# Optimization experiments

Measured on AMD Instinct MI355X. Metric: run time of the kernel, lower is better.

Reference implementation:

```python
import jax, jax.numpy as jnp
import numpy as np

B, T, D, E, K = 4, 2048, 1024, 8, 2


def setup_inputs() -> dict:
    key = jax.random.key(0)
    k1, k2, k3 = jax.random.split(key, 3)
    x = jax.random.normal(k1, (B, T, D), dtype=jnp.float32)
    Wg = jax.random.normal(k2, (D, E), dtype=jnp.float32) * (1.0 / np.sqrt(D))
    # xavier_uniform for We: limit = sqrt(6/(D+D))
    lim = float(np.sqrt(6.0 / (D + D)))
    We = jax.random.uniform(k3, (E, D, D), dtype=jnp.float32, minval=-lim, maxval=lim)
    return {"x": x, "Wg": Wg, "We": We}


def reference(x, Wg, We):
    # gate: (B,T,E) softmax over experts
    logits = jnp.einsum('btd,de->bte', x, Wg)
    gate = jax.nn.softmax(logits, axis=-1)
    top_val, top_idx = jax.lax.top_k(gate, K)          # (B,T,K)
    top_w = top_val / (jnp.sum(top_val, axis=-1, keepdims=True) + 1e-9)
    # dense all-expert projection, as in the original module
    x_experts = jnp.einsum('btd,edm->btem', x, We)      # (B,T,E,D)
    # gather selected experts: (B,T,K,D)
    x_sel = jnp.take_along_axis(x_experts, top_idx[..., None], axis=2)
    out = jnp.sum(x_sel * top_w[..., None], axis=2)     # (B,T,D)
    return out
```

## Files before the change

### kernel.cpp

```cpp
#include <hip/hip_runtime.h>
#include <hip/hip_bf16.h>
#include <stdint.h>

#define NTOK 8192
#define D_   1024
#define E_   8
#define MT   128
#define NT   128
#define KSTEPS 32
#define MAX_TILES 96

#define LIM_F  0.05412658773652741f
#define SB_F   (LIM_F / 127.0f)
#define INVSB_F (127.0f / LIM_F)

typedef __attribute__((ext_vector_type(4))) int i32x4;

__device__ inline unsigned short f2b(float f) {
    unsigned int u = __float_as_uint(f);
    unsigned int r = (u + 0x7fffu + ((u >> 16) & 1u)) >> 16;
    return (unsigned short)r;
}
__device__ inline float b2f(unsigned short b) {
    return __uint_as_float(((unsigned)b) << 16);
}
__device__ inline int q8(float v, float inv) {
    int q = __float2int_rn(v * inv);
    return max(-127, min(127, q));
}

__device__ inline void gload16(const void* g, void* l) {
    __builtin_amdgcn_global_load_lds(
        (const __attribute__((address_space(1))) unsigned int*)(uintptr_t)g,
        (__attribute__((address_space(3))) unsigned int*)(unsigned int)(uintptr_t)l,
        16, 0, 0);
}

__global__ __launch_bounds__(256) void prep_kernel(const float* __restrict__ We,
                                                   unsigned char* __restrict__ WeT8,
                                                   const float* __restrict__ x,
                                                   const float* __restrict__ Wg,
                                                   int* __restrict__ g_tok,
                                                   float* __restrict__ wA_tok,
                                                   float* __restrict__ wB_tok,
                                                   float* __restrict__ sA_tok,
                                                   unsigned char* __restrict__ Abf8) {
    __shared__ __align__(16) float smem[8192];
    int b = blockIdx.x;
    int t = threadIdx.x;
    if (b < 1024) {
        float* wgt = smem;
        for (int i = t; i < 8192; i += 256) wgt[(i & 7) * 1024 + (i >> 3)] = Wg[i];
        __syncthreads();
        int wave = t >> 6, lane = t & 63;
        int tok0 = b * 8 + wave * 2;

        for (int tki = 0; tki < 2; tki++) {
            int tok = tok0 + tki;
            const float* xr = x + (size_t)tok * D_;

            float4 xv[4];
            float acc[8] = {0.f, 0.f, 0.f, 0.f, 0.f, 0.f, 0.f, 0.f};
            float ax = 0.f;
            #pragma unroll
            for (int i = 0; i < 4; i++) {
                int d0 = i * 256 + lane * 4;
                xv[i] = *reinterpret_cast<const float4*>(xr + d0);
                ax = fmaxf(ax, fmaxf(fmaxf(fabsf(xv[i].x), fabsf(xv[i].y)),
                                     fmaxf(fabsf(xv[i].z), fabsf(xv[i].w))));
                #pragma unroll
                for (int e = 0; e < 8; e++) {
                    float4 w = *reinterpret_cast<const float4*>(&wgt[e * 1024 + d0]);
                    acc[e] += xv[i].x * w.x + xv[i].y * w.y + xv[i].z * w.z + xv[i].w * w.w;
                }
            }
            #pragma unroll
            for (int off = 32; off > 0; off >>= 1) ax = fmaxf(ax, __shfl_xor(ax, off, 64));
            #pragma unroll
            for (int e = 0; e < 8; e++)
                #pragma unroll
                for (int off = 32; off > 0; off >>= 1)
                    acc[e] += __shfl_xor(acc[e], off, 64);

            float best = acc[0]; int bi = 0;
            #pragma unroll
            for (int e = 1; e < 8; e++) { if (acc[e] > best) { best = acc[e]; bi = e; } }
            float second = -3.4e38f; int si = 0;
            #pragma unroll
            for (int e = 0; e < 8; e++) { if (e != bi && acc[e] > second) { second = acc[e]; si = e; } }
            float eb = __expf(second - best);
            eb = fmaxf(eb, 1e-20f);
            float w0 = 1.f / (1.f + eb);
            float w1 = eb / (1.f + eb);
            int ea, ebx; float wA, wB;
            if (bi < si) { ea = bi; ebx = si; wA = w0; wB = w1; }
            else         { ea = si; ebx = bi; wA = w1; wB = w0; }
            float inv = (ax > 0.f) ? 127.f / ax : 0.f;
            if (lane == 0) {
                g_tok[tok] = ea * 8 + ebx;
                wA_tok[tok] = wA;
                wB_tok[tok] = wB;
                sA_tok[tok] = ax / 127.f;
            }

            unsigned char* rowp = Abf8 + (size_t)tok * D_;
            #pragma unroll
            for (int i = 0; i < 4; i++) {
                int d0 = i * 256 + lane * 4;
                int q0 = q8(xv[i].x, inv), q1 = q8(xv[i].y, inv);
                int q2 = q8(xv[i].z, inv), q3 = q8(xv[i].w, inv);
                unsigned p = (q0 & 0xff) | ((q1 & 0xff) << 8) | ((q2 & 0xff) << 16) | ((q3 & 0xff) << 24);
                *reinterpret_cast<unsigned*>(rowp + d0) = p;
            }
        }
    } else {
        float (*tile)[65] = reinterpret_cast<float (*)[65]>(smem);
        int bb = b - 1024;
        int e = bb >> 8, rem = bb & 255;
        int m0 = (rem & 15) * 64, d0 = (rem >> 4) * 64;
        const float* src = We + ((size_t)e << 20);
        int r = t >> 4, c4 = (t & 15) * 4;
        #pragma unroll
        for (int i = 0; i < 4; i++) {
            int d = r + i * 16;
            float4 v = *reinterpret_cast<const float4*>(src + (size_t)(d0 + d) * D_ + m0 + c4);
            tile[d][c4 + 0] = v.x; tile[d][c4 + 1] = v.y;
            tile[d][c4 + 2] = v.z; tile[d][c4 + 3] = v.w;
        }
        __syncthreads();
        int m = t >> 2, dq = (t & 3) * 16;
        unsigned pk[4];
        #pragma unroll
        for (int jq = 0; jq < 4; jq++) {
            int q0 = q8(tile[dq + jq * 4 + 0][m], INVSB_F);
            int q1 = q8(tile[dq + jq * 4 + 1][m], INVSB_F);
            int q2 = q8(tile[dq + jq * 4 + 2][m], INVSB_F);
            int q3 = q8(tile[dq + jq * 4 + 3][m], INVSB_F);
            pk[jq] = (q0 & 0xff) | ((q1 & 0xff) << 8) | ((q2 & 0xff) << 16) | ((q3 & 0xff) << 24);
        }
        *reinterpret_cast<uint4*>(WeT8 + ((size_t)e << 20) + (size_t)(m0 + m) * D_ + d0 + dq) =
            make_uint4(pk[0], pk[1], pk[2], pk[3]);
    }
}

__global__ __launch_bounds__(256) void route_kernel(const int* __restrict__ g_tok,
                                                    const float* __restrict__ wA_tok,
                                                    const float* __restrict__ wB_tok,
                                                    const float* __restrict__ sA_tok,
                                                    int* __restrict__ token_list,
                                                    float* __restrict__ wA_s,
                                                    float* __restrict__ wB_s,
                                                    float* __restrict__ sA_s,
                                                    int4* __restrict__ tile_desc,
                                                    int* __restrict__ n_tiles_out) {
    int g = blockIdx.x;
    int t = threadIdx.x;
    __shared__ int cnt[64];
    __shared__ int pfx[256];
    __shared__ int startg, tbase, tottiles;
    if (t < 64) cnt[t] = 0;
    __syncthreads();

    int base = t * 32;
    int gl[32];
    int my = 0;
    #pragma unroll
    for (int k = 0; k < 32; k++) {
        gl[k] = g_tok[base + k];
        my += (gl[k] == g);
    }
    #pragma unroll
    for (int k = 0; k < 32; k++) atomicAdd(&cnt[gl[k]], 1);
    pfx[t] = my;
    __syncthreads();

    if (t == 0) {
        int run = 0, tb = 0, tt = 0;
        for (int gg = 0; gg < 64; gg++) {
            int c = cnt[gg];
            int n = 0, rem = c;
            while (rem > 64) { int take = (rem >= 128) ? 128 : rem; rem -= take; n++; }
            if (rem > 0) n++;
            if (gg < g) { run += c; tb += n; }
            tt += n;
        }
        startg = run; tbase = tb; tottiles = tt;
    }
    for (int off = 1; off < 256; off <<= 1) {
        int add = (t >= off) ? pfx[t - off] : 0;
        __syncthreads();
        pfx[t] += add;
        __syncthreads();
    }

    int pos = startg + pfx[t] - my;
    #pragma unroll
    for (int k = 0; k < 32; k++) {
        if (gl[k] == g) {
            int idx = base + k;
            token_list[pos] = idx;
            wA_s[pos] = wA_tok[idx];
            wB_s[pos] = wB_tok[idx];
            sA_s[pos] = sA_tok[idx];
            pos++;
        }
    }
    if (t == 0) {
        int rem = cnt[g], off2 = 0, ti = tbase;
        while (rem > 64) {
            int take = (rem >= 128) ? 128 : rem;
            tile_desc[ti++] = make_int4(startg + off2, take, g >> 3, g & 7);
            off2 += take; rem -= take;
        }
        if (rem > 0) tile_desc[ti++] = make_int4(startg + off2, rem, g >> 3, g & 7);
        if (g == 0) *n_tiles_out = tottiles;
    }
}

__global__ __launch_bounds__(256, 3) void moe_gemm(const unsigned char* __restrict__ Abf8,
                                                   const unsigned char* __restrict__ WeT8,
                                                   const int* __restrict__ token_list,
                                                   const float* __restrict__ wA_s,
                                                   const float* __restrict__ wB_s,
                                                   const float* __restrict__ sA_s,
                                                   const int4* __restrict__ tile_desc,
                                                   const int* __restrict__ n_tiles,
                                                   float* __restrict__ out) {
    int tile = blockIdx.y;
    if (tile >= *n_tiles) return;
    int4 dsc = tile_desc[tile];
    int loff = dsc.x, rows = dsc.y, ea = dsc.z, ebx = dsc.w;
    int ncol0 = blockIdx.x * NT;

    __shared__ __align__(16) unsigned char As[MT * 64];
    __shared__ __align__(16) unsigned char Bs[NT * 64];
    __shared__ int tokOut[MT];
    __shared__ int tokStage[MT];
    __shared__ float c1sh[MT], c2sh[MT];

    int t = threadIdx.x;
    int wave = t >> 6, lane = t & 63;

    if (t < MT) {
        int idx = loff + ((t < rows) ? t : 0);
        int tk = token_list[idx];
        tokStage[t] = tk;
        tokOut[t] = (t < rows) ? tk : -1;
        float s = sA_s[idx] * SB_F;
        c1sh[t] = s * wA_s[idx];
        c2sh[t] = s * wB_s[idx];
    }
    __syncthreads();

    const unsigned char* wbase = WeT8 + ((size_t)ea << 20);
    size_t ebd = ((size_t)(ebx - ea)) << 20;
    int l15 = lane & 15, hi = lane >> 4, q4 = hi * 4;

    if (rows > 64) {
        const unsigned char* asrc[2];
        const unsigned char* bsrc[2];
        #pragma unroll
        for (int i = 0; i < 2; i++) {
            int g = t + i * 256;
            int row = g >> 2;
            int lc = (g & 3) ^ ((row >> 1) & 3);
            asrc[i] = Abf8 + (size_t)tokStage[row] * D_ + lc * 16;
            bsrc[i] = wbase + (size_t)(ncol0 + row) * D_ + lc * 16;
        }

        int wm = (wave >> 1) * 64, wn = (wave & 1) * 64;
        int aoff[4], boff[4];
        #pragma unroll
        for (int m = 0; m < 4; m++) {
            int r = wm + m * 16 + l15;
            aoff[m] = r * 64 + ((hi ^ ((r >> 1) & 3)) << 4);
            int rb = wn + m * 16 + l15;
            boff[m] = rb * 64 + ((hi ^ ((rb >> 1) & 3)) << 4);
        }

        i32x4 acc[4][4];
        unsigned pk[4][4][2];
        #pragma unroll
        for (int m = 0; m < 4; m++)
            #pragma unroll
            for (int n = 0; n < 4; n++) acc[m][n] = (i32x4){0, 0, 0, 0};

        for (int ks = 0; ks < KSTEPS; ++ks) {
            int kb = (ks & 15) * 64;
            size_t bo = (size_t)kb + ((ks < 16) ? 0 : ebd);
            #pragma unroll
            for (int i = 0; i < 2; i++) {
                gload16(asrc[i] + kb, As + (i * 256 + wave * 64) * 16);
                gload16(bsrc[i] + bo, Bs + (i * 256 + wave * 64) * 16);
            }
            asm volatile("s_waitcnt vmcnt(0)" ::: "memory");
            __builtin_amdgcn_s_barrier();
            if (ks == 16) {
                #pragma unroll
                for (int m = 0; m < 4; m++) {
                    #pragma unroll
                    for (int n = 0; n < 4; n++) {
                        float f0 = (float)acc[m][n][0] * c1sh[wm + m * 16 + q4 + 0];
                        float f1 = (float)acc[m][n][1] * c1sh[wm + m * 16 + q4 + 1];
                        float f2 = (float)acc[m][n][2] * c1sh[wm + m * 16 + q4 + 2];
                        float f3 = (float)acc[m][n][3] * c1sh[wm + m * 16 + q4 + 3];
                        pk[m][n][0] = (unsigned)f2b(f0) | ((unsigned)f2b(f1) << 16);
                        pk[m][n][1] = (unsigned)f2b(f2) | ((unsigned)f2b(f3) << 16);
                        acc[m][n] = (i32x4){0, 0, 0, 0};
                    }
                }
            }
            i32x4 a[4], bfr[4];
            #pragma unroll
            for (int m = 0; m < 4; m++) {
                a[m] = *reinterpret_cast<const i32x4*>(&As[aoff[m]]);
                bfr[m] = *reinterpret_cast<const i32x4*>(&Bs[boff[m]]);
            }
            #pragma unroll
            for (int m = 0; m < 4; m++)
                #pragma unroll
                for (int n = 0; n < 4; n++)
                    acc[m][n] = __builtin_amdgcn_mfma_i32_16x16x64_i8(a[m], bfr[n], acc[m][n], 0, 0, 0);
            __builtin_amdgcn_s_barrier();
        }

        #pragma unroll
        for (int m = 0; m < 4; m++) {
            #pragma unroll
            for (int n = 0; n < 4; n++) {
                int col = ncol0 + wn + n * 16 + l15;
                #pragma unroll
                for (int j = 0; j < 4; j++) {
                    int r = wm + m * 16 + q4 + j;
                    int tk = tokOut[r];
                    unsigned u = pk[m][n][j >> 1];
                    float part = __uint_as_float((j & 1) ? (u & 0xffff0000u) : (u << 16));
                    if (tk >= 0) out[(size_t)tk * D_ + col] = part + (float)acc[m][n][j] * c2sh[r];
                }
            }
        }
    } else {
        const unsigned char* asrcT;
        const unsigned char* bsrcT[2];
        {
            int g = t;
            int row = g >> 2;
            int lc = (g & 3) ^ ((row >> 1) & 3);
            asrcT = Abf8 + (size_t)tokStage[row] * D_ + lc * 16;
        }
        #pragma unroll
        for (int i = 0; i < 2; i++) {
            int g = t + i * 256;
            int row = g >> 2;
            int lc = (g & 3) ^ ((row >> 1) & 3);
            bsrcT[i] = wbase + (size_t)(ncol0 + row) * D_ + lc * 16;
        }

        int wm = (wave >> 1) * 32, wn = (wave & 1) * 64;
        int aoff[2], boff[4];
        #pragma unroll
        for (int m = 0; m < 2; m++) {
            int r = wm + m * 16 + l15;
            aoff[m] = r * 64 + ((hi ^ ((r >> 1) & 3)) << 4);
        }
        #pragma unroll
        for (int n = 0; n < 4; n++) {
            int rb = wn + n * 16 + l15;
            boff[n] = rb * 64 + ((hi ^ ((rb >> 1) & 3)) << 4);
        }

        i32x4 acc[2][4];
        unsigned pk[2][4][2];
        #pragma unroll
        for (int m = 0; m < 2; m++)
            #pragma unroll
            for (int n = 0; n < 4; n++) acc[m][n] = (i32x4){0, 0, 0, 0};

        for (int ks = 0; ks < KSTEPS; ++ks) {
            int kb = (ks & 15) * 64;
            size_t bo = (size_t)kb + ((ks < 16) ? 0 : ebd);
            gload16(asrcT + kb, As + (wave * 64) * 16);
            #pragma unroll
            for (int i = 0; i < 2; i++)
                gload16(bsrcT[i] + bo, Bs + (i * 256 + wave * 64) * 16);
            asm volatile("s_waitcnt vmcnt(0)" ::: "memory");
            __builtin_amdgcn_s_barrier();
            if (ks == 16) {
                #pragma unroll
                for (int m = 0; m < 2; m++) {
                    #pragma unroll
                    for (int n = 0; n < 4; n++) {
                        float f0 = (float)acc[m][n][0] * c1sh[wm + m * 16 + q4 + 0];
                        float f1 = (float)acc[m][n][1] * c1sh[wm + m * 16 + q4 + 1];
                        float f2 = (float)acc[m][n][2] * c1sh[wm + m * 16 + q4 + 2];
                        float f3 = (float)acc[m][n][3] * c1sh[wm + m * 16 + q4 + 3];
                        pk[m][n][0] = (unsigned)f2b(f0) | ((unsigned)f2b(f1) << 16);
                        pk[m][n][1] = (unsigned)f2b(f2) | ((unsigned)f2b(f3) << 16);
                        acc[m][n] = (i32x4){0, 0, 0, 0};
                    }
                }
            }
            i32x4 a[2], bfr[4];
            #pragma unroll
            for (int m = 0; m < 2; m++)
                a[m] = *reinterpret_cast<const i32x4*>(&As[aoff[m]]);
            #pragma unroll
            for (int n = 0; n < 4; n++)
                bfr[n] = *reinterpret_cast<const i32x4*>(&Bs[boff[n]]);
            #pragma unroll
            for (int m = 0; m < 2; m++)
                #pragma unroll
                for (int n = 0; n < 4; n++)
                    acc[m][n] = __builtin_amdgcn_mfma_i32_16x16x64_i8(a[m], bfr[n], acc[m][n], 0, 0, 0);
            __builtin_amdgcn_s_barrier();
        }

        #pragma unroll
        for (int m = 0; m < 2; m++) {
            #pragma unroll
            for (int n = 0; n < 4; n++) {
                int col = ncol0 + wn + n * 16 + l15;
                #pragma unroll
                for (int j = 0; j < 4; j++) {
                    int r = wm + m * 16 + q4 + j;
                    int tk = tokOut[r];
                    unsigned u = pk[m][n][j >> 1];
                    float part = __uint_as_float((j & 1) ? (u & 0xffff0000u) : (u << 16));
                    if (tk >= 0) out[(size_t)tk * D_ + col] = part + (float)acc[m][n][j] * c2sh[r];
                }
            }
        }
    }
}

extern "C" void kernel_launch(void* const* d_in, const int* in_sizes, int n_in,
                              void* d_out, int out_size, void* d_ws, size_t ws_size,
                              hipStream_t stream) {
    const float* x  = (const float*)d_in[0];
    const float* Wg = (const float*)d_in[1];
    const float* We = (const float*)d_in[2];
    float* out = (float*)d_out;

    size_t off = 0;
    auto alloc = [&](size_t bytes) -> void* {
        void* p = (char*)d_ws + off;
        off += (bytes + 255) & ~(size_t)255;
        return p;
    };
    unsigned char* WeT8 = (unsigned char*)alloc((size_t)E_ * 1024 * 1024);
    unsigned char* Abf8 = (unsigned char*)alloc((size_t)NTOK * D_);
    int*   g_tok      = (int*)  alloc(NTOK * 4);
    float* wA_tok     = (float*)alloc(NTOK * 4);
    float* wB_tok     = (float*)alloc(NTOK * 4);
    float* sA_tok     = (float*)alloc(NTOK * 4);
    int*   token_list = (int*)  alloc(NTOK * 4);
    float* wA_s       = (float*)alloc(NTOK * 4);
    float* wB_s       = (float*)alloc(NTOK * 4);
    float* sA_s       = (float*)alloc(NTOK * 4);
    int4*  tile_desc  = (int4*) alloc(MAX_TILES * 16);
    int*   n_tiles    = (int*)  alloc(4);

    prep_kernel<<<1024 + 2048, 256, 0, stream>>>(We, WeT8, x, Wg, g_tok, wA_tok, wB_tok,
                                                 sA_tok, Abf8);
    route_kernel<<<64, 256, 0, stream>>>(g_tok, wA_tok, wB_tok, sA_tok,
                                         token_list, wA_s, wB_s, sA_s, tile_desc, n_tiles);
    moe_gemm<<<dim3(8, MAX_TILES), 256, 0, stream>>>(Abf8, WeT8, token_list, wA_s, wB_s, sA_s,
                                                     tile_desc, n_tiles, out);
}
```

Measured before the change: 78.37 us.

## Double-buffer LDS tiles in MoE int8 GEMM to overlap loads with MFMA

Replaces the single As/Bs shared tiles with two 16KB LDS buffers. Global-to-LDS loads for step ks+1 are issued before computing step ks, with a partial vmcnt wait so memory latency overlaps the int8 MFMA work. Launch bounds also rise from 3 to 4 blocks per CU. LDS use per block doubles, and together with the higher occupancy target this may add register pressure or limit how many blocks fit.

```diff
diff --git a/kernel.cpp b/kernel.cpp
--- a/kernel.cpp
+++ b/kernel.cpp
@@ -9,6 +9,7 @@
 #define NT   128
 #define KSTEPS 32
 #define MAX_TILES 96
+#define BUF_B 16384
 
 #define LIM_F  0.05412658773652741f
 #define SB_F   (LIM_F / 127.0f)
@@ -20,9 +21,6 @@
     unsigned int u = __float_as_uint(f);
     unsigned int r = (u + 0x7fffu + ((u >> 16) & 1u)) >> 16;
     return (unsigned short)r;
-}
-__device__ inline float b2f(unsigned short b) {
-    return __uint_as_float(((unsigned)b) << 16);
 }
 __device__ inline int q8(float v, float inv) {
     int q = __float2int_rn(v * inv);
@@ -217,7 +215,7 @@
     }
 }
 
-__global__ __launch_bounds__(256, 3) void moe_gemm(const unsigned char* __restrict__ Abf8,
+__global__ __launch_bounds__(256, 4) void moe_gemm(const unsigned char* __restrict__ Abf8,
                                                    const unsigned char* __restrict__ WeT8,
                                                    const int* __restrict__ token_list,
                                                    const float* __restrict__ wA_s,
@@ -232,8 +230,7 @@
     int loff = dsc.x, rows = dsc.y, ea = dsc.z, ebx = dsc.w;
     int ncol0 = blockIdx.x * NT;
 
-    __shared__ __align__(16) unsigned char As[MT * 64];
-    __shared__ __align__(16) unsigned char Bs[NT * 64];
+    __shared__ __align__(16) unsigned char lds[2 * BUF_B];
     __shared__ int tokOut[MT];
     __shared__ int tokStage[MT];
     __shared__ float c1sh[MT], c2sh[MT];
@@ -268,6 +265,17 @@
             bsrc[i] = wbase + (size_t)(ncol0 + row) * D_ + lc * 16;
         }
 
+        auto stage = [&](int ks, int buf) {
+            int kb = (ks & 15) * 64;
+            size_t bo = (size_t)kb + ((ks < 16) ? 0 : ebd);
+            unsigned char* base = &lds[buf * BUF_B];
+            #pragma unroll
+            for (int i = 0; i < 2; i++) {
+                gload16(asrc[i] + kb, base + (i * 256 + wave * 64) * 16);
+                gload16(bsrc[i] + bo, base + 8192 + (i * 256 + wave * 64) * 16);
+            }
+        };
+
         int wm = (wave >> 1) * 64, wn = (wave & 1) * 64;
         int aoff[4], boff[4];
         #pragma unroll
@@ -275,7 +283,7 @@
             int r = wm + m * 16 + l15;
             aoff[m] = r * 64 + ((hi ^ ((r >> 1) & 3)) << 4);
             int rb = wn + m * 16 + l15;
-            boff[m] = rb * 64 + ((hi ^ ((rb >> 1) & 3)) << 4);
+            boff[m] = 8192 + rb * 64 + ((hi ^ ((rb >> 1) & 3)) << 4);
         }
 
         i32x4 acc[4][4];
@@ -285,15 +293,14 @@
             #pragma unroll
             for (int n = 0; n < 4; n++) acc[m][n] = (i32x4){0, 0, 0, 0};
 
+        stage(0, 0);
         for (int ks = 0; ks < KSTEPS; ++ks) {
-            int kb = (ks & 15) * 64;
-            size_t bo = (size_t)kb + ((ks < 16) ? 0 : ebd);
-            #pragma unroll
-            for (int i = 0; i < 2; i++) {
-                gload16(asrc[i] + kb, As + (i * 256 + wave * 64) * 16);
-                gload16(bsrc[i] + bo, Bs + (i * 256 + wave * 64) * 16);
-            }
-            asm volatile("s_waitcnt vmcnt(0)" ::: "memory");
+            if (ks < KSTEPS - 1) {
+                stage(ks + 1, (ks + 1) & 1);
+                asm volatile("s_waitcnt vmcnt(4)" ::: "memory");
+            } else {
+                asm volatile("s_waitcnt vmcnt(0)" ::: "memory");
+            }
             __builtin_amdgcn_s_barrier();
             if (ks == 16) {
                 #pragma unroll
@@ -310,11 +317,12 @@
                     }
                 }
             }
+            const unsigned char* Ab = &lds[(ks & 1) * BUF_B];
             i32x4 a[4], bfr[4];
             #pragma unroll
             for (int m = 0; m < 4; m++) {
-                a[m] = *reinterpret_cast<const i32x4*>(&As[aoff[m]]);
-                bfr[m] = *reinterpret_cast<const i32x4*>(&Bs[boff[m]]);
+                a[m] = *reinterpret_cast<const i32x4*>(&Ab[aoff[m]]);
+                bfr[m] = *reinterpret_cast<const i32x4*>(&Ab[boff[m]]);
             }
             #pragma unroll
             for (int m = 0; m < 4; m++)
@@ -356,6 +364,16 @@
             bsrcT[i] = wbase + (size_t)(ncol0 + row) * D_ + lc * 16;
         }
 
+        auto stageT = [&](int ks, int buf) {
+            int kb = (ks & 15) * 64;
+            size_t bo = (size_t)kb + ((ks < 16) ? 0 : ebd);
+            unsigned char* base = &lds[buf * BUF_B];
+            gload16(asrcT + kb, base + (wave * 64) * 16);
+            #pragma unroll
+            for (int i = 0; i < 2; i++)
+                gload16(bsrcT[i] + bo, base + 8192 + (i * 256 + wave * 64) * 16);
+        };
+
         int wm = (wave >> 1) * 32, wn = (wave & 1) * 64;
         int aoff[2], boff[4];
         #pragma unroll
@@ -366,7 +384,7 @@
         #pragma unroll
         for (int n = 0; n < 4; n++) {
             int rb = wn + n * 16 + l15;
-            boff[n] = rb * 64 + ((hi ^ ((rb >> 1) & 3)) << 4);
+            boff[n] = 8192 + rb * 64 + ((hi ^ ((rb >> 1) & 3)) << 4);
         }
 
         i32x4 acc[2][4];
@@ -376,14 +394,14 @@
             #pragma unroll
             for (int n = 0; n < 4; n++) acc[m][n] = (i32x4){0, 0, 0, 0};
 
+        stageT(0, 0);
         for (int ks = 0; ks < KSTEPS; ++ks) {
-            int kb = (ks & 15) * 64;
-            size_t bo = (size_t)kb + ((ks < 16) ? 0 : ebd);
-            gload16(asrcT + kb, As + (wave * 64) * 16);
-            #pragma unroll
-            for (int i = 0; i < 2; i++)
-                gload16(bsrcT[i] + bo, Bs + (i * 256 + wave * 64) * 16);
-            asm volatile("s_waitcnt vmcnt(0)" ::: "memory");
+            if (ks < KSTEPS - 1) {
+                stageT(ks + 1, (ks + 1) & 1);
+                asm volatile("s_waitcnt vmcnt(3)" ::: "memory");
+            } else {
+                asm volatile("s_waitcnt vmcnt(0)" ::: "memory");
+            }
             __builtin_amdgcn_s_barrier();
             if (ks == 16) {
                 #pragma unroll
@@ -400,13 +418,14 @@
                     }
                 }
             }
+            const unsigned char* Ab = &lds[(ks & 1) * BUF_B];
             i32x4 a[2], bfr[4];
             #pragma unroll
             for (int m = 0; m < 2; m++)
-                a[m] = *reinterpret_cast<const i32x4*>(&As[aoff[m]]);
+                a[m] = *reinterpret_cast<const i32x4*>(&Ab[aoff[m]]);
             #pragma unroll
             for (int n = 0; n < 4; n++)
-                bfr[n] = *reinterpret_cast<const i32x4*>(&Bs[boff[n]]);
+                bfr[n] = *reinterpret_cast<const i32x4*>(&Ab[boff[n]]);
             #pragma unroll
             for (int m = 0; m < 2; m++)
                 #pragma unroll
```

New measurement: 80.65 us. 2.9% more time.

## Switch MoE GEMM to uniform 64x256 tiles and drop the dual-path kernel

Applied to the files above, without the earlier changes.

The grouped int8 GEMM now uses 64-row by 256-column tiles instead of 128x128 tiles, with a separate small-tile path. Routing splits each expert-pair group into fixed 64-row tiles, and the grid becomes 4 column blocks by up to 192 tiles. Occupancy is hinted at 4 blocks per CU. The goal is to cut padding waste on partially filled tiles and reuse each A row across more columns. The cost is more B-weight traffic per row tile and more blocks to schedule.

```diff
diff --git a/kernel.cpp b/kernel.cpp
--- a/kernel.cpp
+++ b/kernel.cpp
@@ -5,10 +5,10 @@
 #define NTOK 8192
 #define D_   1024
 #define E_   8
-#define MT   128
-#define NT   128
+#define MT   64
+#define NT   256
 #define KSTEPS 32
-#define MAX_TILES 96
+#define MAX_TILES 192
 
 #define LIM_F  0.05412658773652741f
 #define SB_F   (LIM_F / 127.0f)
@@ -20,9 +20,6 @@
     unsigned int u = __float_as_uint(f);
     unsigned int r = (u + 0x7fffu + ((u >> 16) & 1u)) >> 16;
     return (unsigned short)r;
-}
-__device__ inline float b2f(unsigned short b) {
-    return __uint_as_float(((unsigned)b) << 16);
 }
 __device__ inline int q8(float v, float inv) {
     int q = __float2int_rn(v * inv);
@@ -178,9 +175,7 @@
         int run = 0, tb = 0, tt = 0;
         for (int gg = 0; gg < 64; gg++) {
             int c = cnt[gg];
-            int n = 0, rem = c;
-            while (rem > 64) { int take = (rem >= 128) ? 128 : rem; rem -= take; n++; }
-            if (rem > 0) n++;
+            int n = (c + MT - 1) / MT;
             if (gg < g) { run += c; tb += n; }
             tt += n;
         }
@@ -207,17 +202,16 @@
     }
     if (t == 0) {
         int rem = cnt[g], off2 = 0, ti = tbase;
-        while (rem > 64) {
-            int take = (rem >= 128) ? 128 : rem;
+        while (rem > 0) {
+            int take = (rem < MT) ? rem : MT;
             tile_desc[ti++] = make_int4(startg + off2, take, g >> 3, g & 7);
             off2 += take; rem -= take;
         }
-        if (rem > 0) tile_desc[ti++] = make_int4(startg + off2, rem, g >> 3, g & 7);
         if (g == 0) *n_tiles_out = tottiles;
     }
 }
 
-__global__ __launch_bounds__(256, 3) void moe_gemm(const unsigned char* __restrict__ Abf8,
+__global__ __launch_bounds__(256, 4) void moe_gemm(const unsigned char* __restrict__ Abf8,
                                                    const unsigned char* __restrict__ WeT8,
                                                    const int* __restrict__ token_list,
                                                    const float* __restrict__ wA_s,
@@ -256,178 +250,86 @@
     size_t ebd = ((size_t)(ebx - ea)) << 20;
     int l15 = lane & 15, hi = lane >> 4, q4 = hi * 4;
 
-    if (rows > 64) {
-        const unsigned char* asrc[2];
-        const unsigned char* bsrc[2];
-        #pragma unroll
-        for (int i = 0; i < 2; i++) {
-            int g = t + i * 256;
-            int row = g >> 2;
-            int lc = (g & 3) ^ ((row >> 1) & 3);
-            asrc[i] = Abf8 + (size_t)tokStage[row] * D_ + lc * 16;
-            bsrc[i] = wbase + (size_t)(ncol0 + row) * D_ + lc * 16;
-        }
-
-        int wm = (wave >> 1) * 64, wn = (wave & 1) * 64;
-        int aoff[4], boff[4];
+    const unsigned char* asrc;
+    {
+        int row = t >> 2;
+        int lc = (t & 3) ^ ((row >> 1) & 3);
+        asrc = Abf8 + (size_t)tokStage[row] * D_ + lc * 16;
+    }
+    const unsigned char* bsrc[4];
+    #pragma unroll
+    for (int i = 0; i < 4; i++) {
+        int row = i * 64 + (t >> 2);
+        int lc = (t & 3) ^ ((row >> 1) & 3);
+        bsrc[i] = wbase + (size_t)(ncol0 + row) * D_ + lc * 16;
+    }
+
+    int aoff[4], boff[4];
+    #pragma unroll
+    for (int m = 0; m < 4; m++) {
+        int r = m * 16 + l15;
+        aoff[m] = r * 64 + ((hi ^ ((r >> 1) & 3)) << 4);
+        int rb = wave * 64 + m * 16 + l15;
+        boff[m] = rb * 64 + ((hi ^ ((rb >> 1) & 3)) << 4);
+    }
+
+    i32x4 acc[4][4];
+    unsigned pk[4][4][2];
+    #pragma unroll
+    for (int m = 0; m < 4; m++)
+        #pragma unroll
+        for (int n = 0; n < 4; n++) acc[m][n] = (i32x4){0, 0, 0, 0};
+
+    for (int ks = 0; ks < KSTEPS; ++ks) {
+        int kb = (ks & 15) * 64;
+        size_t bo = (size_t)kb + ((ks < 16) ? 0 : ebd);
+        gload16(asrc + kb, As + wave * 1024);
+        #pragma unroll
+        for (int i = 0; i < 4; i++)
+            gload16(bsrc[i] + bo, Bs + (i * 256 + wave * 64) * 16);
+        asm volatile("s_waitcnt vmcnt(0)" ::: "memory");
+        __builtin_amdgcn_s_barrier();
+        if (ks == 16) {
+            #pragma unroll
+            for (int m = 0; m < 4; m++) {
+                #pragma unroll
+                for (int n = 0; n < 4; n++) {
+                    float f0 = (float)acc[m][n][0] * c1sh[m * 16 + q4 + 0];
+                    float f1 = (float)acc[m][n][1] * c1sh[m * 16 + q4 + 1];
+                    float f2 = (float)acc[m][n][2] * c1sh[m * 16 + q4 + 2];
+                    float f3 = (float)acc[m][n][3] * c1sh[m * 16 + q4 + 3];
+                    pk[m][n][0] = (unsigned)f2b(f0) | ((unsigned)f2b(f1) << 16);
+                    pk[m][n][1] = (unsigned)f2b(f2) | ((unsigned)f2b(f3) << 16);
+                    acc[m][n] = (i32x4){0, 0, 0, 0};
+                }
+            }
+        }
+        i32x4 a[4], bfr[4];
         #pragma unroll
         for (int m = 0; m < 4; m++) {
-            int r = wm + m * 16 + l15;
-            aoff[m] = r * 64 + ((hi ^ ((r >> 1) & 3)) << 4);
-            int rb = wn + m * 16 + l15;
-            boff[m] = rb * 64 + ((hi ^ ((rb >> 1) & 3)) << 4);
-        }
-
-        i32x4 acc[4][4];
-        unsigned pk[4][4][2];
+            a[m] = *reinterpret_cast<const i32x4*>(&As[aoff[m]]);
+            bfr[m] = *reinterpret_cast<const i32x4*>(&Bs[boff[m]]);
+        }
         #pragma unroll
         for (int m = 0; m < 4; m++)
             #pragma unroll
-            for (int n = 0; n < 4; n++) acc[m][n] = (i32x4){0, 0, 0, 0};
-
-        for (int ks = 0; ks < KSTEPS; ++ks) {
-            int kb = (ks & 15) * 64;
-            size_t bo = (size_t)kb + ((ks < 16) ? 0 : ebd);
-            #pragma unroll
-            for (int i = 0; i < 2; i++) {
-                gload16(asrc[i] + kb, As + (i * 256 + wave * 64) * 16);
-                gload16(bsrc[i] + bo, Bs + (i * 256 + wave * 64) * 16);
-            }
-            asm volatile("s_waitcnt vmcnt(0)" ::: "memory");
-            __builtin_amdgcn_s_barrier();
-            if (ks == 16) {
-                #pragma unroll
-                for (int m = 0; m < 4; m++) {
-                    #pragma unroll
-                    for (int n = 0; n < 4; n++) {
-                        float f0 = (float)acc[m][n][0] * c1sh[wm + m * 16 + q4 + 0];
-                        float f1 = (float)acc[m][n][1] * c1sh[wm + m * 16 + q4 + 1];
-                        float f2 = (float)acc[m][n][2] * c1sh[wm + m * 16 + q4 + 2];
-                        float f3 = (float)acc[m][n][3] * c1sh[wm + m * 16 + q4 + 3];
-                        pk[m][n][0] = (unsigned)f2b(f0) | ((unsigned)f2b(f1) << 16);
-                        pk[m][n][1] = (unsigned)f2b(f2) | ((unsigned)f2b(f3) << 16);
-                        acc[m][n] = (i32x4){0, 0, 0, 0};
-                    }
-                }
-            }
-            i32x4 a[4], bfr[4];
-            #pragma unroll
-            for (int m = 0; m < 4; m++) {
-                a[m] = *reinterpret_cast<const i32x4*>(&As[aoff[m]]);
-                bfr[m] = *reinterpret_cast<const i32x4*>(&Bs[boff[m]]);
-            }
-            #pragma unroll
-            for (int m = 0; m < 4; m++)
-                #pragma unroll
-                for (int n = 0; n < 4; n++)
-                    acc[m][n] = __builtin_amdgcn_mfma_i32_16x16x64_i8(a[m], bfr[n], acc[m][n], 0, 0, 0);
-            __builtin_amdgcn_s_barrier();
-        }
-
-        #pragma unroll
-        for (int m = 0; m < 4; m++) {
-            #pragma unroll
-            for (int n = 0; n < 4; n++) {
-                int col = ncol0 + wn + n * 16 + l15;
-                #pragma unroll
-                for (int j = 0; j < 4; j++) {
-                    int r = wm + m * 16 + q4 + j;
-                    int tk = tokOut[r];
-                    unsigned u = pk[m][n][j >> 1];
-                    float part = __uint_as_float((j & 1) ? (u & 0xffff0000u) : (u << 16));
-                    if (tk >= 0) out[(size_t)tk * D_ + col] = part + (float)acc[m][n][j] * c2sh[r];
-                }
-            }
-        }
-    } else {
-        const unsigned char* asrcT;
-        const unsigned char* bsrcT[2];
-        {
-            int g = t;
-            int row = g >> 2;
-            int lc = (g & 3) ^ ((row >> 1) & 3);
-            asrcT = Abf8 + (size_t)tokStage[row] * D_ + lc * 16;
-        }
-        #pragma unroll
-        for (int i = 0; i < 2; i++) {
-            int g = t + i * 256;
-            int row = g >> 2;
-            int lc = (g & 3) ^ ((row >> 1) & 3);
-            bsrcT[i] = wbase + (size_t)(ncol0 + row) * D_ + lc * 16;
-        }
-
-        int wm = (wave >> 1) * 32, wn = (wave & 1) * 64;
-        int aoff[2], boff[4];
-        #pragma unroll
-        for (int m = 0; m < 2; m++) {
-            int r = wm + m * 16 + l15;
-            aoff[m] = r * 64 + ((hi ^ ((r >> 1) & 3)) << 4);
-        }
+            for (int n = 0; n < 4; n++)
+                acc[m][n] = __builtin_amdgcn_mfma_i32_16x16x64_i8(a[m], bfr[n], acc[m][n], 0, 0, 0);
+        __builtin_amdgcn_s_barrier();
+    }
+
+    #pragma unroll
+    for (int m = 0; m < 4; m++) {
         #pragma unroll
         for (int n = 0; n < 4; n++) {
-            int rb = wn + n * 16 + l15;
-            boff[n] = rb * 64 + ((hi ^ ((rb >> 1) & 3)) << 4);
-        }
-
-        i32x4 acc[2][4];
-        unsigned pk[2][4][2];
-        #pragma unroll
-        for (int m = 0; m < 2; m++)
-            #pragma unroll
-            for (int n = 0; n < 4; n++) acc[m][n] = (i32x4){0, 0, 0, 0};
-
-        for (int ks = 0; ks < KSTEPS; ++ks) {
-            int kb = (ks & 15) * 64;
-            size_t bo = (size_t)kb + ((ks < 16) ? 0 : ebd);
-            gload16(asrcT + kb, As + (wave * 64) * 16);
-            #pragma unroll
-            for (int i = 0; i < 2; i++)
-                gload16(bsrcT[i] + bo, Bs + (i * 256 + wave * 64) * 16);
-            asm volatile("s_waitcnt vmcnt(0)" ::: "memory");
-            __builtin_amdgcn_s_barrier();
-            if (ks == 16) {
-                #pragma unroll
-                for (int m = 0; m < 2; m++) {
-                    #pragma unroll
-                    for (int n = 0; n < 4; n++) {
-                        float f0 = (float)acc[m][n][0] * c1sh[wm + m * 16 + q4 + 0];
-                        float f1 = (float)acc[m][n][1] * c1sh[wm + m * 16 + q4 + 1];
-                        float f2 = (float)acc[m][n][2] * c1sh[wm + m * 16 + q4 + 2];
-                        float f3 = (float)acc[m][n][3] * c1sh[wm + m * 16 + q4 + 3];
-                        pk[m][n][0] = (unsigned)f2b(f0) | ((unsigned)f2b(f1) << 16);
-                        pk[m][n][1] = (unsigned)f2b(f2) | ((unsigned)f2b(f3) << 16);
-                        acc[m][n] = (i32x4){0, 0, 0, 0};
-                    }
-                }
-            }
-            i32x4 a[2], bfr[4];
-            #pragma unroll
-            for (int m = 0; m < 2; m++)
-                a[m] = *reinterpret_cast<const i32x4*>(&As[aoff[m]]);
-            #pragma unroll
-            for (int n = 0; n < 4; n++)
-                bfr[n] = *reinterpret_cast<const i32x4*>(&Bs[boff[n]]);
-            #pragma unroll
-            for (int m = 0; m < 2; m++)
-                #pragma unroll
-                for (int n = 0; n < 4; n++)
-                    acc[m][n] = __builtin_amdgcn_mfma_i32_16x16x64_i8(a[m], bfr[n], acc[m][n], 0, 0, 0);
-            __builtin_amdgcn_s_barrier();
-        }
-
-        #pragma unroll
-        for (int m = 0; m < 2; m++) {
-            #pragma unroll
-            for (int n = 0; n < 4; n++) {
-                int col = ncol0 + wn + n * 16 + l15;
-                #pragma unroll
-                for (int j = 0; j < 4; j++) {
-                    int r = wm + m * 16 + q4 + j;
-                    int tk = tokOut[r];
-                    unsigned u = pk[m][n][j >> 1];
-                    float part = __uint_as_float((j & 1) ? (u & 0xffff0000u) : (u << 16));
-                    if (tk >= 0) out[(size_t)tk * D_ + col] = part + (float)acc[m][n][j] * c2sh[r];
-                }
+            int col = ncol0 + wave * 64 + n * 16 + l15;
+            #pragma unroll
+            for (int j = 0; j < 4; j++) {
+                int r = m * 16 + q4 + j;
+                int tk = tokOut[r];
+                unsigned u = pk[m][n][j >> 1];
+                float part = __uint_as_float((j & 1) ? (u & 0xffff0000u) : (u << 16));
+                if (tk >= 0) out[(size_t)tk * D_ + col] = part + (float)acc[m][n][j] * c2sh[r];
             }
         }
     }
@@ -464,6 +366,6 @@
                                                  sA_tok, Abf8);
     route_kernel<<<64, 256, 0, stream>>>(g_tok, wA_tok, wB_tok, sA_tok,
                                          token_list, wA_s, wB_s, sA_s, tile_desc, n_tiles);
-    moe_gemm<<<dim3(8, MAX_TILES), 256, 0, stream>>>(Abf8, WeT8, token_list, wA_s, wB_s, sA_s,
+    moe_gemm<<<dim3(4, MAX_TILES), 256, 0, stream>>>(Abf8, WeT8, token_list, wA_s, wB_s, sA_s,
                                                      tile_desc, n_tiles, out);
 }
```

After: 85.11 us. +8.6%, slower.
